# Optimization experiments

Measured on AMD Instinct MI355X. Metric: run time of the kernel, lower is better.

The kernel has to match this reference:

```python
import jax, jax.numpy as jnp
import numpy as np

N, CIN, COUT, K, S, H, W = 16, 512, 512, 3, 512, 64, 64
EPS = 1e-8


def setup_inputs() -> dict:
    key = jax.random.key(0)
    k1, k2, k3, k4 = jax.random.split(key, 4)
    return {
        "x": jax.random.normal(k1, (N, CIN, H, W), jnp.float32),
        "style": jax.random.normal(k2, (N, S), jnp.float32),
        # conv weight ~ N(0,1) as in the torch module (lr_mul=1)
        "weight": jax.random.normal(k3, (COUT, CIN, K, K), jnp.float32),
        # style modulation linear: weight ~ N(0,1), bias init 1.0
        "style_w": jax.random.normal(k4, (CIN, S), jnp.float32),
        "style_b": jnp.ones((CIN,), jnp.float32),
    }


def reference(x, style, weight, style_w, style_b):
    # equalized-lr scales (gain=1.0, lr_mul=1.0, mode=fan_in)
    lin_scale = 1.0 / jnp.sqrt(jnp.float32(S))          # fan_in of linear = style_channels
    w_scale = 1.0 / jnp.sqrt(jnp.float32(CIN * K * K))  # fan_in of weight[0] = Cin*k*k

    # style modulation: s[n, cin] (style_bias = 0.0)
    s = style @ (style_w.T * lin_scale) + style_b        # [N, Cin]

    w = weight * w_scale                                  # [Cout, Cin, K, K]

    # demodulation: rsqrt(sum_{i,kh,kw} (w[o,i]*s[n,i])^2 + eps) per (n, o)
    demod = jax.lax.rsqrt(jnp.einsum('oikl,ni->no', w * w, s * s) + EPS)  # [N, Cout]

    # fused form: conv(x * s, W) * demod  ==  grouped conv with per-sample modulated weights
    xs = x * s[:, :, None, None]
    out = jax.lax.conv_general_dilated(
        xs, w, window_strides=(1, 1), padding='SAME',
        dimension_numbers=('NCHW', 'OIHW', 'NCHW'))
    return out * demod[:, :, None, None]
```

## Files before the change

### kernel.cpp

```cpp
#include <hip/hip_runtime.h>
#include <hip/hip_bf16.h>

#define CIN   512
#define COUT  512
#define HW    4096
#define PADW  66
#define NB    16

static constexpr float LIN_SCALE = 0.044194173824159216f;
static constexpr float W_SCALE   = 0.014731391274719738f;

typedef __attribute__((ext_vector_type(8))) short bf16x8;
typedef __attribute__((ext_vector_type(4))) float f32x4;

__device__ __forceinline__ unsigned short f2us(float f) {
    __hip_bfloat16 h = __float2bfloat16(f); unsigned short u; __builtin_memcpy(&u, &h, 2); return u;
}

typedef const __attribute__((address_space(1))) unsigned int guint;
typedef __attribute__((address_space(3))) unsigned int luint;
__device__ __forceinline__ void gload_lds16(const void* g, void* l) {
    __builtin_amdgcn_global_load_lds((guint*)g, (luint*)l, 16, 0, 0);
}

__global__ void k_style(const float* __restrict__ style,
                        const float* __restrict__ style_w,
                        const float* __restrict__ style_b,
                        float* __restrict__ s) {
    int wid  = (blockIdx.x * blockDim.x + threadIdx.x) >> 6;
    int lane = threadIdx.x & 63;
    int n = wid >> 9, i = wid & 511;
    float sum = 0.f;
    for (int j = lane; j < 512; j += 64)
        sum += style[n * 512 + j] * style_w[i * 512 + j];
    for (int m = 32; m; m >>= 1) sum += __shfl_xor(sum, m, 64);
    if (lane == 0) s[n * 512 + i] = sum * LIN_SCALE + style_b[i];
}

__global__ void k_wprep(const float* __restrict__ weight,
                        float* __restrict__ wsq,
                        __hip_bfloat16* __restrict__ wt) {
    int oi = blockIdx.x * 256 + threadIdx.x;
    float sq = 0.f;
#pragma unroll
    for (int tp = 0; tp < 9; ++tp) {
        float v = weight[(size_t)oi * 9 + tp] * W_SCALE;
        sq += v * v;
        wt[(size_t)tp * (COUT * CIN) + oi] = __float2bfloat16(v);
    }
    wsq[oi] = sq;
}

__global__ void k_demod(const float* __restrict__ wsq, const float* __restrict__ s,
                        float* __restrict__ demod) {
    int wid  = (blockIdx.x * blockDim.x + threadIdx.x) >> 6;
    int lane = threadIdx.x & 63;
    int n = wid >> 9, o = wid & 511;
    float sum = 0.f;
    for (int i = lane; i < 512; i += 64) {
        float sv = s[n * 512 + i];
        sum += wsq[o * 512 + i] * sv * sv;
    }
    for (int m = 32; m; m >>= 1) sum += __shfl_xor(sum, m, 64);
    if (lane == 0) demod[n * 512 + o] = rsqrtf(sum + 1e-8f);
}

__global__ void k_border(__hip_bfloat16* __restrict__ xs) {
    int bp = blockIdx.x, n = blockIdx.y, t = threadIdx.x;
    int hp, wp;
    if (bp < 66)       { hp = 0;  wp = bp; }
    else if (bp < 132) { hp = 65; wp = bp - 66; }
    else { int k2 = bp - 132; hp = 1 + (k2 >> 1); wp = (k2 & 1) ? 65 : 0; }
    uint4 z = make_uint4(0u, 0u, 0u, 0u);
    *(uint4*)(xs + (((size_t)n * PADW * PADW) + hp * PADW + wp) * 512 + t * 8) = z;
}

__global__ void k_xs(const float* __restrict__ x, const float* __restrict__ s,
                     __hip_bfloat16* __restrict__ xs) {
    const int h = blockIdx.x;
    const int n = blockIdx.y;
    const int t = threadIdx.x;
    const int PITCH = 66;
    __shared__ float lds[64 * 66];
    for (int ic = 0; ic < 8; ++ic) {
        const int i0 = ic * 64;
        __syncthreads();
#pragma unroll
        for (int j = 0; j < 4; ++j) {
            int idx = j * 256 + t;
            int il = idx >> 4;
            int wq = (idx & 15) * 4;
            float4 v = *(const float4*)(x + (((size_t)n * 512 + i0 + il) * HW) + h * 64 + wq);
            float* dst = &lds[il * PITCH + wq];
            dst[0] = v.x; dst[1] = v.y; dst[2] = v.z; dst[3] = v.w;
        }
        __syncthreads();
#pragma unroll
        for (int j = 0; j < 2; ++j) {
            int idx = j * 256 + t;
            int wp = idx >> 3;
            int ib = (idx & 7) * 8;
            unsigned short tmp[8];
#pragma unroll
            for (int r = 0; r < 8; ++r) {
                float xv = lds[(ib + r) * PITCH + wp];
                float sv = s[n * 512 + i0 + ib + r];
                tmp[r] = f2us(xv * sv);
            }
            uint4 o;
            o.x = (unsigned)tmp[0] | ((unsigned)tmp[1] << 16);
            o.y = (unsigned)tmp[2] | ((unsigned)tmp[3] << 16);
            o.z = (unsigned)tmp[4] | ((unsigned)tmp[5] << 16);
            o.w = (unsigned)tmp[6] | ((unsigned)tmp[7] << 16);
            *(uint4*)(xs + ((size_t)((n * PADW + h + 1) * PADW + (wp + 1))) * 512 + i0 + ib) = o;
        }
    }
}

__global__ __launch_bounds__(256) void k_conv(
        const __hip_bfloat16* __restrict__ wt,
        const __hip_bfloat16* __restrict__ xs,
        const float* __restrict__ demod,
        float* __restrict__ out) {
    __shared__ char lds[32768];
    const int tid = threadIdx.x;
    const int wave = tid >> 6, lane = tid & 63;
    const int tN = blockIdx.x;
    const int o0 = blockIdx.y * 128;
    const int n  = blockIdx.z;

    const int cb = (lane & 7) * 8;
    size_t Aoff[4], Boff[4];
#pragma unroll
    for (int j = 0; j < 4; ++j) {
        const int r = wave * 32 + j * 8 + (lane >> 3);
        Aoff[j] = (size_t)(o0 + r) * CIN + cb;
        const int hw0 = tN * 128 + r;
        Boff[j] = ((size_t)(hw0 >> 6) * PADW + (hw0 & 63)) * CIN + cb;
    }
    const __hip_bfloat16* xsn = xs + (size_t)n * PADW * PADW * CIN;

    char* ldsA = lds + wave * 4096;
    char* ldsB = lds + 16384 + wave * 4096;

    const int qd = lane >> 4, col = lane & 15;
    const char* aRd = lds + (((wave & 1) * 64 + col) * 128) + qd * 16;
    const char* bRd = lds + 16384 + (((wave >> 1) * 64 + col) * 128) + qd * 16;

    f32x4 acc[4][4] = {};

    for (int tp = 0; tp < 9; ++tp) {
        const size_t tapA = (size_t)tp * (COUT * CIN);
        const int kh = tp / 3, kw = tp % 3;
        const size_t tapB = ((size_t)kh * PADW + kw) * CIN;
        for (int c = 0; c < 8; ++c) {
            __syncthreads();
#pragma unroll
            for (int j = 0; j < 4; ++j) {
                gload_lds16(wt  + tapA + Aoff[j] + c * 64, ldsA + j * 1024);
                gload_lds16(xsn + tapB + Boff[j] + c * 64, ldsB + j * 1024);
            }
            __syncthreads();
#pragma unroll
            for (int kk = 0; kk < 2; ++kk) {
                bf16x8 af[4], bfr[4];
#pragma unroll
                for (int mt = 0; mt < 4; ++mt)
                    af[mt] = *(const bf16x8*)(aRd + mt * 16 * 128 + kk * 64);
#pragma unroll
                for (int nt = 0; nt < 4; ++nt)
                    bfr[nt] = *(const bf16x8*)(bRd + nt * 16 * 128 + kk * 64);
#pragma unroll
                for (int mt = 0; mt < 4; ++mt)
#pragma unroll
                    for (int nt = 0; nt < 4; ++nt)
                        acc[mt][nt] = __builtin_amdgcn_mfma_f32_16x16x32_bf16(
                            af[mt], bfr[nt], acc[mt][nt], 0, 0, 0);
            }
        }
    }

    const int oBase  = o0 + (wave & 1) * 64;
    const int hwBase = tN * 128 + (wave >> 1) * 64 + col;
#pragma unroll
    for (int mt = 0; mt < 4; ++mt) {
#pragma unroll
        for (int rg = 0; rg < 4; ++rg) {
            const int o = oBase + mt * 16 + qd * 4 + rg;
            const float dm = demod[n * 512 + o];
            float* orow = out + ((size_t)(n * COUT + o)) * HW + hwBase;
#pragma unroll
            for (int nt = 0; nt < 4; ++nt)
                orow[nt * 16] = acc[mt][nt][rg] * dm;
        }
    }
}

extern "C" void kernel_launch(void* const* d_in, const int* in_sizes, int n_in,
                              void* d_out, int out_size, void* d_ws, size_t ws_size,
                              hipStream_t stream) {
    const float* x       = (const float*)d_in[0];
    const float* style   = (const float*)d_in[1];
    const float* weight  = (const float*)d_in[2];
    const float* style_w = (const float*)d_in[3];
    const float* style_b = (const float*)d_in[4];
    float* out = (float*)d_out;

    char* ws = (char*)d_ws;
    float*          s_buf  = (float*)(ws + 0);
    float*          wsq    = (float*)(ws + 32768);
    float*          demod  = (float*)(ws + 1081344);
    __hip_bfloat16* wt     = (__hip_bfloat16*)(ws + 1114112);
    __hip_bfloat16* xs     = (__hip_bfloat16*)(ws + 5832704);

    k_style <<<dim3(2048),     dim3(256), 0, stream>>>(style, style_w, style_b, s_buf);
    k_wprep <<<dim3(1024),     dim3(256), 0, stream>>>(weight, wsq, wt);
    k_demod <<<dim3(2048),     dim3(256), 0, stream>>>(wsq, s_buf, demod);
    k_border<<<dim3(260, 16),  dim3(64),  0, stream>>>(xs);
    k_xs    <<<dim3(64, 16),   dim3(256), 0, stream>>>(x, s_buf, xs);
    k_conv  <<<dim3(32, 4, 16), dim3(256), 0, stream>>>(wt, xs, demod, out);
}
```

Before: 587.7 us.

## Rewrite conv GEMM with 256x256 tiles, double-buffered LDS and XCD-aware mapping

The implicit-GEMM conv kernel now uses 512-thread blocks computing 256x256 output tiles. Global-to-LDS loads for the next K step are interleaved with MFMA work on the current step, and LDS is double-buffered. LDS addresses are XOR-swizzled to avoid bank conflicts, weights are relaid out as [Cout][tap*Cin] so the K dimension is contiguous, and block IDs are mapped so each XCD handles particular samples for L2 locality. This aims to hide memory latency and raise MFMA utilisation over the previous single-buffered 128x128 kernel. The cost is heavy register pressure from 32 accumulator tiles and fragile hand-placed waitcnt and barrier ordering.

Result: faster. 503.3 us (-14.4%).

```diff
diff --git a/kernel.cpp b/kernel.cpp
--- a/kernel.cpp
+++ b/kernel.cpp
@@ -6,6 +6,9 @@
 #define HW    4096
 #define PADW  66
 #define NB    16
+#define KTOT  4608
+#define BUFSZ 65536
+#define BOFF  32768
 
 static constexpr float LIN_SCALE = 0.044194173824159216f;
 static constexpr float W_SCALE   = 0.014731391274719738f;
@@ -41,12 +44,13 @@
                         float* __restrict__ wsq,
                         __hip_bfloat16* __restrict__ wt) {
     int oi = blockIdx.x * 256 + threadIdx.x;
+    int o = oi >> 9, i = oi & 511;
     float sq = 0.f;
 #pragma unroll
     for (int tp = 0; tp < 9; ++tp) {
         float v = weight[(size_t)oi * 9 + tp] * W_SCALE;
         sq += v * v;
-        wt[(size_t)tp * (COUT * CIN) + oi] = __float2bfloat16(v);
+        wt[(size_t)o * KTOT + tp * 512 + i] = __float2bfloat16(v);
     }
     wsq[oi] = sq;
 }
@@ -117,81 +121,135 @@
     }
 }
 
-__global__ __launch_bounds__(256) void k_conv(
+#define BAR      __builtin_amdgcn_s_barrier()
+#define WAITLGKM asm volatile("s_waitcnt lgkmcnt(0)" ::: "memory")
+#define LOAD_B(CH) { _Pragma("unroll") for (int t_ = 0; t_ < 4; ++t_) \
+    bfr[t_] = *(const bf16x8*)(cb + BOFF + bRow + t_ * 2048 + (CH)); }
+#define LOAD_A(MG, CH) { _Pragma("unroll") for (int t_ = 0; t_ < 4; ++t_) \
+    af[t_] = *(const bf16x8*)(cb + aRow + ((MG) * 4 + t_) * 2048 + (CH)); }
+#define DO_MFMA(MG) { __builtin_amdgcn_s_setprio(1); \
+    _Pragma("unroll") for (int m_ = 0; m_ < 4; ++m_) \
+    _Pragma("unroll") for (int n_ = 0; n_ < 4; ++n_) \
+        acc[(MG) * 4 + m_][n_] = __builtin_amdgcn_mfma_f32_16x16x32_bf16( \
+            af[m_], bfr[n_], acc[(MG) * 4 + m_][n_], 0, 0, 0); \
+    __builtin_amdgcn_s_setprio(0); }
+
+__global__ __launch_bounds__(512, 2) void k_conv(
         const __hip_bfloat16* __restrict__ wt,
         const __hip_bfloat16* __restrict__ xs,
         const float* __restrict__ demod,
         float* __restrict__ out) {
-    __shared__ char lds[32768];
-    const int tid = threadIdx.x;
-    const int wave = tid >> 6, lane = tid & 63;
-    const int tN = blockIdx.x;
-    const int o0 = blockIdx.y * 128;
-    const int n  = blockIdx.z;
-
-    const int cb = (lane & 7) * 8;
-    size_t Aoff[4], Boff[4];
-#pragma unroll
-    for (int j = 0; j < 4; ++j) {
-        const int r = wave * 32 + j * 8 + (lane >> 3);
-        Aoff[j] = (size_t)(o0 + r) * CIN + cb;
-        const int hw0 = tN * 128 + r;
-        Boff[j] = ((size_t)(hw0 >> 6) * PADW + (hw0 & 63)) * CIN + cb;
-    }
-    const __hip_bfloat16* xsn = xs + (size_t)n * PADW * PADW * CIN;
-
-    char* ldsA = lds + wave * 4096;
-    char* ldsB = lds + 16384 + wave * 4096;
-
-    const int qd = lane >> 4, col = lane & 15;
-    const char* aRd = lds + (((wave & 1) * 64 + col) * 128) + qd * 16;
-    const char* bRd = lds + 16384 + (((wave >> 1) * 64 + col) * 128) + qd * 16;
-
-    f32x4 acc[4][4] = {};
-
-    for (int tp = 0; tp < 9; ++tp) {
-        const size_t tapA = (size_t)tp * (COUT * CIN);
-        const int kh = tp / 3, kw = tp % 3;
-        const size_t tapB = ((size_t)kh * PADW + kw) * CIN;
-        for (int c = 0; c < 8; ++c) {
-            __syncthreads();
-#pragma unroll
-            for (int j = 0; j < 4; ++j) {
-                gload_lds16(wt  + tapA + Aoff[j] + c * 64, ldsA + j * 1024);
-                gload_lds16(xsn + tapB + Boff[j] + c * 64, ldsB + j * 1024);
-            }
-            __syncthreads();
-#pragma unroll
-            for (int kk = 0; kk < 2; ++kk) {
-                bf16x8 af[4], bfr[4];
-#pragma unroll
-                for (int mt = 0; mt < 4; ++mt)
-                    af[mt] = *(const bf16x8*)(aRd + mt * 16 * 128 + kk * 64);
-#pragma unroll
-                for (int nt = 0; nt < 4; ++nt)
-                    bfr[nt] = *(const bf16x8*)(bRd + nt * 16 * 128 + kk * 64);
-#pragma unroll
-                for (int mt = 0; mt < 4; ++mt)
-#pragma unroll
-                    for (int nt = 0; nt < 4; ++nt)
-                        acc[mt][nt] = __builtin_amdgcn_mfma_f32_16x16x32_bf16(
-                            af[mt], bfr[nt], acc[mt][nt], 0, 0, 0);
-            }
-        }
-    }
-
-    const int oBase  = o0 + (wave & 1) * 64;
-    const int hwBase = tN * 128 + (wave >> 1) * 64 + col;
-#pragma unroll
-    for (int mt = 0; mt < 4; ++mt) {
+    __shared__ __attribute__((aligned(16))) char smem[2 * BUFSZ];
+    const int tid  = threadIdx.x;
+    const int wv   = tid >> 6, lane = tid & 63;
+    const int wm   = wv >> 2,  wn   = wv & 3;
+
+    const int bid = blockIdx.x;
+    const int xcd = bid & 7, idx = bid >> 3;
+    const int pT  = idx & 15;
+    const int o0  = ((idx >> 4) & 1) * 256;
+    const int smp = xcd * 2 + (idx >> 5);
+
+    const __hip_bfloat16* xsn = xs + (size_t)smp * (PADW * PADW * 512);
+
+    const int rw = lane >> 3, cl = lane & 7;
+    const int lc = cl ^ rw;
+    const size_t aOff = (size_t)(wv * 8 + rw) * KTOT + lc * 8;
+    const size_t bOff = (size_t)(wv * 8 + rw) * 512  + lc * 8;
+    const __hip_bfloat16* aStage = wt  + (size_t)o0 * KTOT + aOff;
+    const __hip_bfloat16* bStage = xsn + bOff;
+
+    const int col = lane & 15, qd = lane >> 4;
+    const int ch0 = ((qd)     ^ (col & 7)) << 4;
+    const int ch1 = ((qd + 4) ^ (col & 7)) << 4;
+    const int aRow = (wm * 128 + col) * 128;
+    const int bRow = (wn * 64  + col) * 128;
+
+    f32x4 acc[8][4] = {};
+
+    {
+        char* nbB = smem + BOFF + wv * 1024;
+        char* nbA = smem + wv * 1024;
+        const __hip_bfloat16* bS = bStage + (size_t)(pT * 4) * 33792;
+        gload_lds16(bS,              nbB);
+        gload_lds16(bS + 33792,      nbB + 8192);
+        gload_lds16(bS + 2 * 33792,  nbB + 2 * 8192);
+        gload_lds16(bS + 3 * 33792,  nbB + 3 * 8192);
+        gload_lds16(aStage,              nbA);
+        gload_lds16(aStage + 2 * 294912, nbA + 2 * 8192);
+        gload_lds16(aStage + 294912,     nbA + 8192);
+        gload_lds16(aStage + 3 * 294912, nbA + 3 * 8192);
+        asm volatile("s_waitcnt vmcnt(2)" ::: "memory");
+        BAR;
+    }
+
+    for (int kt = 0; kt < 71; ++kt) {
+        char* cb = smem + (kt & 1) * BUFSZ;
+        char* nb = smem + ((kt + 1) & 1) * BUFSZ;
+        const int kt1  = kt + 1;
+        const int tap1 = kt1 >> 3, c1 = kt1 & 7;
+        const int kh1  = tap1 / 3, kw1 = tap1 - kh1 * 3;
+        const __hip_bfloat16* aS = aStage + (size_t)kt1 * 64;
+        const __hip_bfloat16* bS = bStage +
+            (size_t)((pT * 4 + kh1) * PADW + kw1) * 512 + c1 * 64;
+        char* nbB = nb + BOFF + wv * 1024;
+        char* nbA = nb + wv * 1024;
+
+        bf16x8 af[4], bfr[4];
+
+        LOAD_B(ch0); LOAD_A(0, ch0);
+        gload_lds16(bS,             nbB);
+        gload_lds16(bS + 33792,     nbB + 8192);
+        gload_lds16(bS + 2 * 33792, nbB + 2 * 8192);
+        BAR; WAITLGKM;
+        DO_MFMA(0);
+        asm volatile("s_waitcnt vmcnt(3)" ::: "memory");
+        BAR;
+
+        LOAD_A(1, ch0);
+        gload_lds16(bS + 3 * 33792, nbB + 3 * 8192);
+        gload_lds16(aS,             nbA);
+        gload_lds16(aS + 2 * 294912, nbA + 2 * 8192);
+        BAR; WAITLGKM;
+        DO_MFMA(1);
+        BAR;
+
+        LOAD_B(ch1); LOAD_A(0, ch1);
+        gload_lds16(aS + 294912,     nbA + 8192);
+        gload_lds16(aS + 3 * 294912, nbA + 3 * 8192);
+        BAR; WAITLGKM;
+        DO_MFMA(0);
+        BAR;
+
+        LOAD_A(1, ch1);
+        BAR; WAITLGKM;
+        DO_MFMA(1);
+        asm volatile("s_waitcnt vmcnt(2)" ::: "memory");
+        BAR;
+    }
+
+    {
+        char* cb = smem + BUFSZ;
+        asm volatile("s_waitcnt vmcnt(0)" ::: "memory");
+        BAR;
+        bf16x8 af[4], bfr[4];
+        LOAD_B(ch0); LOAD_A(0, ch0); DO_MFMA(0);
+        LOAD_A(1, ch0);              DO_MFMA(1);
+        LOAD_B(ch1); LOAD_A(0, ch1); DO_MFMA(0);
+        LOAD_A(1, ch1);              DO_MFMA(1);
+    }
+
+    const int hwBase = pT * 256 + wn * 64 + col;
+#pragma unroll
+    for (int m = 0; m < 8; ++m) {
 #pragma unroll
         for (int rg = 0; rg < 4; ++rg) {
-            const int o = oBase + mt * 16 + qd * 4 + rg;
-            const float dm = demod[n * 512 + o];
-            float* orow = out + ((size_t)(n * COUT + o)) * HW + hwBase;
-#pragma unroll
-            for (int nt = 0; nt < 4; ++nt)
-                orow[nt * 16] = acc[mt][nt][rg] * dm;
+            const int o = o0 + wm * 128 + m * 16 + qd * 4 + rg;
+            const float dm = demod[smp * 512 + o];
+            float* orow = out + ((size_t)(smp * COUT + o)) * HW + hwBase;
+#pragma unroll
+            for (int nn = 0; nn < 4; ++nn)
+                orow[nn * 16] = acc[m][nn][rg] * dm;
         }
     }
 }
@@ -218,5 +276,5 @@
     k_demod <<<dim3(2048),     dim3(256), 0, stream>>>(wsq, s_buf, demod);
     k_border<<<dim3(260, 16),  dim3(64),  0, stream>>>(xs);
     k_xs    <<<dim3(64, 16),   dim3(256), 0, stream>>>(x, s_buf, xs);
-    k_conv  <<<dim3(32, 4, 16), dim3(256), 0, stream>>>(wt, xs, demod, out);
-}
+    k_conv  <<<dim3(512),      dim3(512), 0, stream>>>(wt, xs, demod, out);
+}
```
